# Performance work log

Measured on AMD Instinct MI355X. Metric: run time of the kernel, lower is better.

The kernel has to match this reference:

```python
import jax, jax.numpy as jnp
import numpy as np

B, S, D = 2, 2048, 2048
E, K, F = 8, 2, 4096
EPS_LN = 1e-5
EPS_AUX = 1e-9


def setup_inputs() -> dict:
    key = jax.random.key(0)
    ks = jax.random.split(key, 12)
    s_d = 1.0 / np.sqrt(D)
    s_f = 1.0 / np.sqrt(F)
    return {
        "x": jax.random.normal(ks[0], (B, S, D), dtype=jnp.float32),
        # router LayerNorm
        "ln_gamma": jnp.ones((D,), jnp.float32),
        "ln_beta": jnp.zeros((D,), jnp.float32),
        # router MLP: Linear(D,D) -> ReLU -> Linear(D,E)
        "rW1": jax.random.uniform(ks[1], (D, D), jnp.float32, -s_d, s_d),
        "rb1": jnp.zeros((D,), jnp.float32),
        "rW2": jax.random.uniform(ks[2], (D, E), jnp.float32, -s_d, s_d),
        "rb2": jnp.zeros((E,), jnp.float32),
        # experts: per-expert FFN D -> F -> D
        "We1": jax.random.uniform(ks[3], (E, D, F), jnp.float32, -s_d, s_d),
        "be1": jnp.zeros((E, F), jnp.float32),
        "We2": jax.random.uniform(ks[4], (E, F, D), jnp.float32, -s_f, s_f),
        "be2": jnp.zeros((E, D), jnp.float32),
    }


def _layer_norm(x, gamma, beta):
    mu = jnp.mean(x, axis=-1, keepdims=True)
    var = jnp.mean(jnp.square(x - mu), axis=-1, keepdims=True)
    return (x - mu) * jax.lax.rsqrt(var + EPS_LN) * gamma + beta


def reference(x, ln_gamma, ln_beta, rW1, rb1, rW2, rb2, We1, be1, We2, be2):
    # --- BaseRouter ---
    x_norm = _layer_norm(x, ln_gamma, ln_beta)
    h = jax.nn.relu(jnp.einsum("bsd,de->bse", x_norm, rW1) + rb1)
    router_logits = jnp.einsum("bsd,de->bse", h, rW2) + rb2  # [B,S,E]
    router_probs = jax.nn.softmax(router_logits, axis=-1)

    top_k_probs, top_k_indices = jax.lax.top_k(router_probs, K)  # [B,S,K]
    top_k_probs = top_k_probs / jnp.sum(top_k_probs, axis=-1, keepdims=True)

    # aux load-balance loss (detached in original via .item())
    p_mean = jnp.mean(router_probs, axis=(0, 1))  # [E]
    aux_loss = jnp.sum(p_mean * jnp.log(p_mean * E + EPS_AUX))

    # --- dispatch / combine weights: scatter top-k probs to [B,S,E] ---
    one_hot = jax.nn.one_hot(top_k_indices, E, dtype=x.dtype)  # [B,S,K,E]
    combine = jnp.einsum("bske,bsk->bse", one_hot, top_k_probs)  # [B,S,E]

    # --- experts: dense per-expert FFN, weighted combine ---
    eh = jax.nn.relu(jnp.einsum("bsd,edf->ebsf", x, We1) + be1[:, None, None, :])
    ey = jnp.einsum("ebsf,efd->ebsd", eh, We2) + be2[:, None, None, :]
    out = jnp.einsum("ebsd,bse->bsd", ey, combine)

    return out, aux_loss
```

## Files before the change

kernel.cpp:

```cpp
#include <hip/hip_runtime.h>
#include <hip/hip_bf16.h>

#define NTOK 4096
#define DIM  2048
#define NEXP 8
#define FDIM 4096
#define NPAIR 8192

typedef __attribute__((ext_vector_type(4))) float     f32x4;
typedef __attribute__((ext_vector_type(8))) short     s16x8;
typedef __attribute__((ext_vector_type(4))) short     s16x4;
typedef __attribute__((ext_vector_type(8))) _Float16  f16x8;
typedef __attribute__((ext_vector_type(4))) _Float16  f16x4;

#define DEVI static __device__ __forceinline__

DEVI void gl2lds(const void* g, void* l) {
  __builtin_amdgcn_global_load_lds((const __attribute__((address_space(1))) unsigned int*)g,
                                   (__attribute__((address_space(3))) unsigned int*)l, 16, 0, 0);
}

DEVI float bf2f(unsigned short s) {
  unsigned int u = ((unsigned int)s) << 16; float f; __builtin_memcpy(&f, &u, 4); return f;
}
DEVI unsigned short f2bf(float f) {
  __hip_bfloat16 h = __float2bfloat16(f); unsigned short s; __builtin_memcpy(&s, &h, 2); return s;
}
DEVI float wredsum(float v) {
#pragma unroll
  for (int o = 32; o > 0; o >>= 1) v += __shfl_xor(v, o);
  return v;
}

__global__ __launch_bounds__(256) void ln_conv_kernel(
    const float* __restrict__ x, const float* __restrict__ gamma, const float* __restrict__ beta,
    _Float16* __restrict__ xh, _Float16* __restrict__ xl, unsigned short* __restrict__ xbf)
{
  int tok = blockIdx.x;
  int tid = threadIdx.x, lane = tid & 63, wv = tid >> 6;
  const float* xr = x + (size_t)tok * DIM;
  float v[8];
  *(float4*)(v)     = *(const float4*)(xr + tid * 8);
  *(float4*)(v + 4) = *(const float4*)(xr + tid * 8 + 4);
  float s = v[0]+v[1]+v[2]+v[3]+v[4]+v[5]+v[6]+v[7];
  __shared__ float red[4];
  s = wredsum(s);
  if (lane == 0) red[wv] = s;
  __syncthreads();
  float mu = (red[0]+red[1]+red[2]+red[3]) * (1.f / DIM);
  __syncthreads();
  float s2 = 0.f;
#pragma unroll
  for (int j = 0; j < 8; j++) { float d = v[j] - mu; s2 += d * d; }
  s2 = wredsum(s2);
  if (lane == 0) red[wv] = s2;
  __syncthreads();
  float var = (red[0]+red[1]+red[2]+red[3]) * (1.f / DIM);
  float rs = 1.0f / sqrtf(var + 1e-5f);

  float4 g0 = *(const float4*)(gamma + tid*8), g1 = *(const float4*)(gamma + tid*8 + 4);
  float4 b0 = *(const float4*)(beta  + tid*8), b1 = *(const float4*)(beta  + tid*8 + 4);
  float gg[8] = {g0.x,g0.y,g0.z,g0.w,g1.x,g1.y,g1.z,g1.w};
  float bb[8] = {b0.x,b0.y,b0.z,b0.w,b1.x,b1.y,b1.z,b1.w};
  f16x8 vh, vl; s16x8 vb;
#pragma unroll
  for (int j = 0; j < 8; j++) {
    float xn = (v[j] - mu) * rs * gg[j] + bb[j];
    _Float16 h = (_Float16)xn;
    vh[j] = h;
    vl[j] = (_Float16)((xn - (float)h) * 4096.f);
    vb[j] = (short)f2bf(v[j]);
  }
  *(f16x8*)(xh + (size_t)tok*DIM + tid*8) = vh;
  *(f16x8*)(xl + (size_t)tok*DIM + tid*8) = vl;
  *(s16x8*)(xbf + (size_t)tok*DIM + tid*8) = vb;
}

__global__ __launch_bounds__(256) void transpose_bf16_kernel(
    const float* __restrict__ src, unsigned short* __restrict__ dst, int R, int C)
{
  src += (size_t)blockIdx.z * R * C;
  dst += (size_t)blockIdx.z * R * C;
  __shared__ float tile[64][65];
  int r0 = blockIdx.y * 64, c0 = blockIdx.x * 64;
  int tx = threadIdx.x & 15, ty = threadIdx.x >> 4;
#pragma unroll
  for (int i = 0; i < 4; i++) {
    float4 v = *(const float4*)(src + (size_t)(r0 + ty*4 + i) * C + c0 + tx*4);
    tile[ty*4+i][tx*4+0] = v.x; tile[ty*4+i][tx*4+1] = v.y;
    tile[ty*4+i][tx*4+2] = v.z; tile[ty*4+i][tx*4+3] = v.w;
  }
  __syncthreads();
#pragma unroll
  for (int i = 0; i < 4; i++) {
    int c = c0 + ty*4 + i;
    s16x4 o;
    o[0] = (short)f2bf(tile[tx*4+0][ty*4+i]); o[1] = (short)f2bf(tile[tx*4+1][ty*4+i]);
    o[2] = (short)f2bf(tile[tx*4+2][ty*4+i]); o[3] = (short)f2bf(tile[tx*4+3][ty*4+i]);
    *(s16x4*)(dst + (size_t)c * R + r0 + tx*4) = o;
  }
}

__global__ __launch_bounds__(256) void transpose_f16split_kernel(
    const float* __restrict__ src, _Float16* __restrict__ dh, _Float16* __restrict__ dl, int R, int C)
{
  __shared__ float tile[64][65];
  int r0 = blockIdx.y * 64, c0 = blockIdx.x * 64;
  int tx = threadIdx.x & 15, ty = threadIdx.x >> 4;
#pragma unroll
  for (int i = 0; i < 4; i++) {
    float4 v = *(const float4*)(src + (size_t)(r0 + ty*4 + i) * C + c0 + tx*4);
    tile[ty*4+i][tx*4+0] = v.x; tile[ty*4+i][tx*4+1] = v.y;
    tile[ty*4+i][tx*4+2] = v.z; tile[ty*4+i][tx*4+3] = v.w;
  }
  __syncthreads();
#pragma unroll
  for (int i = 0; i < 4; i++) {
    int c = c0 + ty*4 + i;
    f16x4 oh, ol;
#pragma unroll
    for (int j = 0; j < 4; j++) {
      float f = tile[tx*4+j][ty*4+i];
      _Float16 h = (_Float16)f;
      oh[j] = h;
      ol[j] = (_Float16)((f - (float)h) * 4096.f);
    }
    *(f16x4*)(dh + (size_t)c * R + r0 + tx*4) = oh;
    *(f16x4*)(dl + (size_t)c * R + r0 + tx*4) = ol;
  }
}

#define R_TA 10240
#define R_TB 5120
__global__ __launch_bounds__(256) void router_gemm_kernel(
    const _Float16* __restrict__ Ah, const _Float16* __restrict__ Al,
    const _Float16* __restrict__ Bh, const _Float16* __restrict__ Bl,
    const float* __restrict__ bias, float* __restrict__ Cout)
{
  __shared__ char lds[2*R_TA + 2*R_TB];
  char* lAh = lds;             char* lAl = lds + R_TA;
  char* lBh = lds + 2*R_TA;    char* lBl = lds + 2*R_TA + R_TB;
  const int K = DIM;
  int m0 = blockIdx.y * 128, n0 = blockIdx.x * 64;
  int tid = threadIdx.x, lane = tid & 63, wv = tid >> 6;
  int wm = wv >> 1, wn = wv & 1;

  const char* srcAh[3]; const char* srcAl[3];
  const char* srcBh[2]; const char* srcBl[2];
  {
    int i = 0;
    for (int c = wv; c < 10; c += 4, i++) {
      int doff = c*1024 + lane*16;
      int row = doff / 80; int b = doff - row*80; if (b >= 64) b = 0;
      srcAh[i] = (const char*)(Ah + (size_t)(m0+row)*K) + b;
      srcAl[i] = (const char*)(Al + (size_t)(m0+row)*K) + b;
    }
    i = 0;
    for (int c = wv; c < 5; c += 4, i++) {
      int doff = c*1024 + lane*16;
      int row = doff / 80; int b = doff - row*80; if (b >= 64) b = 0;
      srcBh[i] = (const char*)(Bh + (size_t)(n0+row)*K) + b;
      srcBl[i] = (const char*)(Bl + (size_t)(n0+row)*K) + b;
    }
  }

  f32x4 acc1[4][2], acc2[4][2];
#pragma unroll
  for (int mb = 0; mb < 4; mb++)
#pragma unroll
    for (int nb = 0; nb < 2; nb++) {
      acc1[mb][nb] = (f32x4){0.f,0.f,0.f,0.f};
      acc2[mb][nb] = (f32x4){0.f,0.f,0.f,0.f};
    }

  for (int kt = 0; kt < K/32; kt++) {
    {
      int i = 0;
      for (int c = wv; c < 10; c += 4, i++) {
        gl2lds(srcAh[i], lAh + c*1024);
        gl2lds(srcAl[i], lAl + c*1024);
        srcAh[i] += 64; srcAl[i] += 64;
      }
      i = 0;
      for (int c = wv; c < 5; c += 4, i++) {
        gl2lds(srcBh[i], lBh + c*1024);
        gl2lds(srcBl[i], lBl + c*1024);
        srcBh[i] += 64; srcBl[i] += 64;
      }
    }
    __syncthreads();
    int kb = (lane >> 4) * 16;
    f16x8 ah[4], al[4], bh[2], bl[2];
#pragma unroll
    for (int mb = 0; mb < 4; mb++) {
      int r = wm*64 + mb*16 + (lane & 15);
      ah[mb] = *(const f16x8*)(lAh + r*80 + kb);
      al[mb] = *(const f16x8*)(lAl + r*80 + kb);
    }
#pragma unroll
    for (int nb = 0; nb < 2; nb++) {
      int r = wn*32 + nb*16 + (lane & 15);
      bh[nb] = *(const f16x8*)(lBh + r*80 + kb);
      bl[nb] = *(const f16x8*)(lBl + r*80 + kb);
    }
#pragma unroll
    for (int mb = 0; mb < 4; mb++)
#pragma unroll
      for (int nb = 0; nb < 2; nb++) {
        acc1[mb][nb] = __builtin_amdgcn_mfma_f32_16x16x32_f16(ah[mb], bh[nb], acc1[mb][nb], 0,0,0);
        acc2[mb][nb] = __builtin_amdgcn_mfma_f32_16x16x32_f16(ah[mb], bl[nb], acc2[mb][nb], 0,0,0);
        acc2[mb][nb] = __builtin_amdgcn_mfma_f32_16x16x32_f16(al[mb], bh[nb], acc2[mb][nb], 0,0,0);
      }
    __syncthreads();
  }
#pragma unroll
  for (int mb = 0; mb < 4; mb++)
#pragma unroll
    for (int nb = 0; nb < 2; nb++) {
      int col = n0 + wn*32 + nb*16 + (lane & 15);
      float bv = bias[col];
#pragma unroll
      for (int r = 0; r < 4; r++) {
        int m = m0 + wm*64 + mb*16 + (lane >> 4)*4 + r;
        float hval = acc1[mb][nb][r] + acc2[mb][nb][r] * (1.f/4096.f) + bv;
        Cout[(size_t)m*DIM + col] = fmaxf(hval, 0.f);
      }
    }
}

__global__ __launch_bounds__(256) void router_logits_kernel(
    const float* __restrict__ h, const float* __restrict__ rW2, const float* __restrict__ rb2,
    float* __restrict__ probs,
    int* __restrict__ eid, float* __restrict__ wts)
{
  int lane = threadIdx.x & 63, wv = threadIdx.x >> 6;
  int tok = blockIdx.x * 4 + wv;
  const float* hr = h + (size_t)tok * DIM;
  float lg[8] = {0,0,0,0,0,0,0,0};
#pragma unroll
  for (int j = 0; j < 8; j++) {
    int k = j * 256 + lane * 4;
    float4 hv = *(const float4*)(hr + k);
    float hv4[4] = {hv.x, hv.y, hv.z, hv.w};
#pragma unroll
    for (int r = 0; r < 4; r++) {
      const float4* w4 = (const float4*)(rW2 + (size_t)(k + r) * NEXP);
      float4 wa = w4[0], wb = w4[1];
      lg[0] += hv4[r]*wa.x; lg[1] += hv4[r]*wa.y; lg[2] += hv4[r]*wa.z; lg[3] += hv4[r]*wa.w;
      lg[4] += hv4[r]*wb.x; lg[5] += hv4[r]*wb.y; lg[6] += hv4[r]*wb.z; lg[7] += hv4[r]*wb.w;
    }
  }
#pragma unroll
  for (int e = 0; e < 8; e++) {
#pragma unroll
    for (int o = 32; o > 0; o >>= 1) lg[e] += __shfl_xor(lg[e], o);
  }
  if (lane == 0) {
    float l[8], p[8];
    float m = -1e30f;
#pragma unroll
    for (int e = 0; e < 8; e++) { l[e] = lg[e] + rb2[e]; m = fmaxf(m, l[e]); }
    float s = 0.f;
#pragma unroll
    for (int e = 0; e < 8; e++) { p[e] = expf(l[e] - m); s += p[e]; }
    float inv = 1.f / s;
#pragma unroll
    for (int e = 0; e < 8; e++) { p[e] *= inv; probs[(size_t)tok*8 + e] = p[e]; }
    int i0 = 0;
#pragma unroll
    for (int e = 1; e < 8; e++) if (p[e] > p[i0]) i0 = e;
    int i1 = (i0 == 0) ? 1 : 0;
#pragma unroll
    for (int e = 0; e < 8; e++) if (e != i0 && p[e] > p[i1]) i1 = e;
    float denom = 1.f / (p[i0] + p[i1]);
    eid[tok*2+0] = i0; eid[tok*2+1] = i1;
    wts[tok*2+0] = p[i0]*denom; wts[tok*2+1] = p[i1]*denom;
  }
}

__global__ __launch_bounds__(256) void router_sort_kernel(
    const int* __restrict__ eid, const float* __restrict__ probs,
    int* __restrict__ cnt, int* __restrict__ basep,
    int* __restrict__ tokenlist, int* __restrict__ pairslot,
    float* __restrict__ aux_out)
{
  __shared__ int hist[256][8];
  __shared__ float wsum[4][8];
  __shared__ int bl[8];
  __shared__ int lcnt[8];
  int t = threadIdx.x, lane = t & 63, wv = t >> 6;

  int me[32];
  {
    const int4* ep = (const int4*)(eid + t * 32);
#pragma unroll
    for (int q = 0; q < 8; q++) {
      int4 v = ep[q];
      me[q*4+0] = v.x; me[q*4+1] = v.y; me[q*4+2] = v.z; me[q*4+3] = v.w;
    }
  }
#pragma unroll
  for (int e = 0; e < 8; e++) {
    int ce = 0;
#pragma unroll
    for (int i = 0; i < 32; i++) ce += (me[i] == e) ? 1 : 0;
    hist[t][e] = ce;
  }

  float part[8] = {0,0,0,0,0,0,0,0};
  for (int i = 0; i < 16; i++) {
    const float4* p4 = (const float4*)(probs + (size_t)(t*16 + i) * 8);
    float4 a = p4[0], b = p4[1];
    part[0]+=a.x; part[1]+=a.y; part[2]+=a.z; part[3]+=a.w;
    part[4]+=b.x; part[5]+=b.y; part[6]+=b.z; part[7]+=b.w;
  }
#pragma unroll
  for (int e = 0; e < 8; e++) {
#pragma unroll
    for (int o = 32; o > 0; o >>= 1) part[e] += __shfl_xor(part[e], o);
  }
  if (lane == 0) {
#pragma unroll
    for (int e = 0; e < 8; e++) wsum[wv][e] = part[e];
  }
  __syncthreads();

  if (t < 8) {
    int running = 0;
    for (int i = 0; i < 256; i++) { int tmp = hist[i][t]; hist[i][t] = running; running += tmp; }
    lcnt[t] = running;
  }
  __syncthreads();
  if (t == 0) {
    int b = 0; float aux = 0.f;
#pragma unroll
    for (int e = 0; e < 8; e++) {
      int ce = lcnt[e];
      bl[e] = b; basep[e] = b; cnt[e] = ce; b += ce;
      float pm = (wsum[0][e]+wsum[1][e]+wsum[2][e]+wsum[3][e]) * (1.f / NTOK);
      aux += pm * logf(pm * 8.f + 1e-9f);
    }
    *aux_out = aux;
  }
  __syncthreads();

#pragma unroll
  for (int i = 0; i < 32; i++) {
    int e = me[i];
    int r = 0;
#pragma unroll
    for (int j = 0; j < i; j++) r += (me[j] == e) ? 1 : 0;
    int slot = bl[e] + hist[t][e] + r;
    int pair = t*32 + i;
    tokenlist[slot] = pair >> 1;
    pairslot[pair] = slot;
  }
}

template<int MODE>
__global__ __launch_bounds__(256, 2) void expert_gemm_v3(
    const unsigned short* __restrict__ Abase,
    const unsigned short* __restrict__ Bbase,
    const float* __restrict__ bias,
    unsigned short* __restrict__ Cout,
    const int* __restrict__ cnt, const int* __restrict__ basep,
    const int* __restrict__ tokenlist)
{
  const int K = (MODE == 1) ? DIM : FDIM;
  const int N = (MODE == 1) ? FDIM : DIM;
  __shared__ char lds[65536];
  int e = blockIdx.y >> 5, mt = blockIdx.y & 31;
  int ne = cnt[e];
  if (mt * 128 >= ne) return;
  int mbase = basep[e] + mt * 128;
  int n0 = blockIdx.x * 128;
  int tid = threadIdx.x, lane = tid & 63, wv = tid >> 6;
  int wm = wv >> 1, wn = wv & 1;

  const char* srcA[4]; const char* srcB[4];
  int sb = (((lane & 7) ^ ((lane >> 3) & 7)) << 4);
#pragma unroll
  for (int i = 0; i < 4; i++) {
    int c = wv + i*4;
    int row = c*8 + (lane >> 3);
    int slot = mbase + row; if (slot > NPAIR - 1) slot = NPAIR - 1;
    size_t arow = (MODE == 1) ? (size_t)tokenlist[slot] : (size_t)slot;
    srcA[i] = (const char*)(Abase + arow * K) + sb;
    srcB[i] = (const char*)(Bbase + ((size_t)e * N + n0 + row) * K) + sb;
  }

  f32x4 acc[4][4];
#pragma unroll
  for (int mb = 0; mb < 4; mb++)
#pragma unroll
    for (int nb = 0; nb < 4; nb++) acc[mb][nb] = (f32x4){0.f,0.f,0.f,0.f};

#pragma unroll
  for (int i = 0; i < 4; i++) {
    gl2lds(srcA[i], lds + (wv + i*4)*1024);
    gl2lds(srcB[i], lds + 16384 + (wv + i*4)*1024);
  }
  asm volatile("s_waitcnt vmcnt(0)\n\ts_barrier" ::: "memory");

  const int NT = K / 64;
  int rsw = (lane & 7) << 4;
  int cur = 0;
  for (int kt = 0; kt < NT; kt++) {
    char* cA = lds + cur*32768;
    char* cB = cA + 16384;
    if (kt + 1 < NT) {
      char* nA = lds + (cur^1)*32768;
      char* nB = nA + 16384;
      size_t ko = (size_t)(kt + 1) * 128;
#pragma unroll
      for (int i = 0; i < 4; i++) {
        gl2lds(srcA[i] + ko, nA + (wv + i*4)*1024);
        gl2lds(srcB[i] + ko, nB + (wv + i*4)*1024);
      }
    }
#pragma unroll
    for (int ks = 0; ks < 2; ks++) {
      int kb = (ks*64 + (lane >> 4)*16) ^ rsw;
      s16x8 af[4], bf[4];
#pragma unroll
      for (int mb = 0; mb < 4; mb++)
        af[mb] = *(const s16x8*)(cA + (wm*64 + mb*16 + (lane & 15))*128 + kb);
#pragma unroll
      for (int nb = 0; nb < 4; nb++)
        bf[nb] = *(const s16x8*)(cB + (wn*64 + nb*16 + (lane & 15))*128 + kb);
#pragma unroll
      for (int mb = 0; mb < 4; mb++)
#pragma unroll
        for (int nb = 0; nb < 4; nb++)
          acc[mb][nb] = __builtin_amdgcn_mfma_f32_16x16x32_bf16(af[mb], bf[nb], acc[mb][nb], 0,0,0);
    }
    __builtin_amdgcn_sched_barrier(0);
    asm volatile("s_waitcnt lgkmcnt(0)\n\ts_waitcnt vmcnt(0)\n\ts_barrier" ::: "memory");
    __builtin_amdgcn_sched_barrier(0);
    cur ^= 1;
  }

#pragma unroll
  for (int mb = 0; mb < 4; mb++)
#pragma unroll
    for (int nb = 0; nb < 4; nb++) {
      int col = n0 + wn*64 + nb*16 + (lane & 15);
      float bv = bias[(size_t)e * N + col];
#pragma unroll
      for (int r = 0; r < 4; r++) {
        int mloc = mt*128 + wm*64 + mb*16 + (lane >> 4)*4 + r;
        if (mloc < ne) {
          float v = acc[mb][nb][r] + bv;
          if (MODE == 1) v = fmaxf(v, 0.f);
          Cout[((size_t)basep[e] + mloc) * N + col] = f2bf(v);
        }
      }
    }
}

__global__ __launch_bounds__(256) void combine_kernel(
    const unsigned short* __restrict__ Yg, const int* __restrict__ pairslot,
    const float* __restrict__ wts, float* __restrict__ out)
{
  int tok = blockIdx.x, tid = threadIdx.x;
  int s0 = pairslot[tok*2], s1 = pairslot[tok*2+1];
  float w0 = wts[tok*2], w1 = wts[tok*2+1];
  s16x8 a = *(const s16x8*)(Yg + (size_t)s0 * DIM + tid*8);
  s16x8 b = *(const s16x8*)(Yg + (size_t)s1 * DIM + tid*8);
  float o[8];
#pragma unroll
  for (int j = 0; j < 8; j++)
    o[j] = w0 * bf2f((unsigned short)a[j]) + w1 * bf2f((unsigned short)b[j]);
  float* op = out + (size_t)tok * DIM + tid*8;
  float4 o0; o0.x=o[0]; o0.y=o[1]; o0.z=o[2]; o0.w=o[3];
  float4 o1; o1.x=o[4]; o1.y=o[5]; o1.z=o[6]; o1.w=o[7];
  *(float4*)op = o0;
  *(float4*)(op + 4) = o1;
}

extern "C" void kernel_launch(void* const* d_in, const int* in_sizes, int n_in,
                              void* d_out, int out_size, void* d_ws, size_t ws_size,
                              hipStream_t stream)
{
  (void)in_sizes; (void)n_in; (void)out_size; (void)ws_size;
  const float* x    = (const float*)d_in[0];
  const float* ln_g = (const float*)d_in[1];
  const float* ln_b = (const float*)d_in[2];
  const float* rW1  = (const float*)d_in[3];
  const float* rb1  = (const float*)d_in[4];
  const float* rW2  = (const float*)d_in[5];
  const float* rb2  = (const float*)d_in[6];
  const float* We1  = (const float*)d_in[7];
  const float* be1  = (const float*)d_in[8];
  const float* We2  = (const float*)d_in[9];
  const float* be2  = (const float*)d_in[10];
  float* out = (float*)d_out;
  float* aux_out = out + (size_t)NTOK * DIM;

  char* ws = (char*)d_ws;
  size_t off = 0;
  auto alloc = [&](size_t bytes) { char* p = ws + off; off += (bytes + 255) & ~(size_t)255; return p; };

  _Float16* XH   = (_Float16*)alloc((size_t)NTOK * DIM * 2);
  _Float16* XL   = (_Float16*)alloc((size_t)NTOK * DIM * 2);
  unsigned short* XBF = (unsigned short*)alloc((size_t)NTOK * DIM * 2);
  _Float16* RW1H = (_Float16*)alloc((size_t)DIM * DIM * 2);
  _Float16* RW1L = (_Float16*)alloc((size_t)DIM * DIM * 2);
  unsigned short* WET = (unsigned short*)alloc((size_t)NEXP * FDIM * DIM * 2);
  unsigned short* EH  = (unsigned short*)alloc((size_t)(NPAIR + 128) * FDIM * 2);
  char* HY = alloc((size_t)(NPAIR + 128) * DIM * 2 > (size_t)NTOK*DIM*4
                     ? (size_t)(NPAIR + 128) * DIM * 2 : (size_t)NTOK*DIM*4);
  float* H = (float*)HY;
  unsigned short* YG = (unsigned short*)HY;
  float* PROB = (float*)alloc((size_t)NTOK * 8 * 4);
  int* CNT  = (int*)alloc(256);
  int* BASE = CNT + 16;
  int* EID  = (int*)alloc((size_t)NPAIR * 4);
  float* WTS = (float*)alloc((size_t)NPAIR * 4);
  int* PAIRSLOT = (int*)alloc((size_t)NPAIR * 4);
  int* TOKLIST  = (int*)alloc((size_t)(NPAIR + 128) * 4);

  ln_conv_kernel<<<NTOK, 256, 0, stream>>>(x, ln_g, ln_b, XH, XL, XBF);
  transpose_f16split_kernel<<<dim3(DIM/64, DIM/64), 256, 0, stream>>>(rW1, RW1H, RW1L, DIM, DIM);
  transpose_bf16_kernel<<<dim3(FDIM/64, DIM/64, NEXP), 256, 0, stream>>>(We1, WET, DIM, FDIM);
  router_gemm_kernel<<<dim3(DIM/64, NTOK/128), 256, 0, stream>>>(XH, XL, RW1H, RW1L, rb1, H);
  router_logits_kernel<<<NTOK/4, 256, 0, stream>>>(H, rW2, rb2, PROB, EID, WTS);
  router_sort_kernel<<<1, 256, 0, stream>>>(EID, PROB, CNT, BASE, TOKLIST, PAIRSLOT, aux_out);
  expert_gemm_v3<1><<<dim3(FDIM/128, NEXP*32), 256, 0, stream>>>(XBF, WET, be1, EH, CNT, BASE, TOKLIST);
  transpose_bf16_kernel<<<dim3(DIM/64, FDIM/64, NEXP), 256, 0, stream>>>(We2, WET, FDIM, DIM);
  expert_gemm_v3<2><<<dim3(DIM/128, NEXP*32), 256, 0, stream>>>(EH, WET, be2, YG, CNT, BASE, TOKLIST);
  combine_kernel<<<NTOK, 256, 0, stream>>>(YG, PAIRSLOT, WTS, out);
}
```

Baseline: 838.8 us.

## Single-buffer expert GEMM LDS and raise occupancy with M-tile-fastest grid

The expert GEMM drops LDS double buffering (64KB to 32KB) and uses plain __syncthreads around each K step, with launch bounds raised to 5 waves per SIMD. The grid is reordered so M-tiles vary fastest and each expert's N-tiles fall along the y dimension. The goal is to hide latency through higher occupancy rather than in-block prefetch, and to improve weight reuse in L2 across concurrent blocks. The cost is that loads are no longer overlapped with MFMA inside a block, and the tighter register budget may spill the 64-float accumulator tile.

Result: slower. 2.153 ms (+156.7%).

```diff
diff --git a/kernel.cpp b/kernel.cpp
--- a/kernel.cpp
+++ b/kernel.cpp
@@ -358,7 +358,7 @@
 }
 
 template<int MODE>
-__global__ __launch_bounds__(256, 2) void expert_gemm_v3(
+__global__ __launch_bounds__(256, 5) void expert_gemm_v4(
     const unsigned short* __restrict__ Abase,
     const unsigned short* __restrict__ Bbase,
     const float* __restrict__ bias,
@@ -368,12 +368,14 @@
 {
   const int K = (MODE == 1) ? DIM : FDIM;
   const int N = (MODE == 1) ? FDIM : DIM;
-  __shared__ char lds[65536];
-  int e = blockIdx.y >> 5, mt = blockIdx.y & 31;
+  const int NTN = N / 128;
+  __shared__ char lds[32768];
+  int mt = blockIdx.x;
+  int e = blockIdx.y / NTN;
+  int n0 = (blockIdx.y % NTN) * 128;
   int ne = cnt[e];
   if (mt * 128 >= ne) return;
   int mbase = basep[e] + mt * 128;
-  int n0 = blockIdx.x * 128;
   int tid = threadIdx.x, lane = tid & 63, wv = tid >> 6;
   int wm = wv >> 1, wn = wv & 1;
 
@@ -395,49 +397,33 @@
 #pragma unroll
     for (int nb = 0; nb < 4; nb++) acc[mb][nb] = (f32x4){0.f,0.f,0.f,0.f};
 
-#pragma unroll
-  for (int i = 0; i < 4; i++) {
-    gl2lds(srcA[i], lds + (wv + i*4)*1024);
-    gl2lds(srcB[i], lds + 16384 + (wv + i*4)*1024);
-  }
-  asm volatile("s_waitcnt vmcnt(0)\n\ts_barrier" ::: "memory");
-
   const int NT = K / 64;
   int rsw = (lane & 7) << 4;
-  int cur = 0;
   for (int kt = 0; kt < NT; kt++) {
-    char* cA = lds + cur*32768;
-    char* cB = cA + 16384;
-    if (kt + 1 < NT) {
-      char* nA = lds + (cur^1)*32768;
-      char* nB = nA + 16384;
-      size_t ko = (size_t)(kt + 1) * 128;
-#pragma unroll
-      for (int i = 0; i < 4; i++) {
-        gl2lds(srcA[i] + ko, nA + (wv + i*4)*1024);
-        gl2lds(srcB[i] + ko, nB + (wv + i*4)*1024);
-      }
-    }
+    size_t ko = (size_t)kt * 128;
+#pragma unroll
+    for (int i = 0; i < 4; i++) {
+      gl2lds(srcA[i] + ko, lds + (wv + i*4)*1024);
+      gl2lds(srcB[i] + ko, lds + 16384 + (wv + i*4)*1024);
+    }
+    __syncthreads();
 #pragma unroll
     for (int ks = 0; ks < 2; ks++) {
       int kb = (ks*64 + (lane >> 4)*16) ^ rsw;
       s16x8 af[4], bf[4];
 #pragma unroll
       for (int mb = 0; mb < 4; mb++)
-        af[mb] = *(const s16x8*)(cA + (wm*64 + mb*16 + (lane & 15))*128 + kb);
+        af[mb] = *(const s16x8*)(lds + (wm*64 + mb*16 + (lane & 15))*128 + kb);
 #pragma unroll
       for (int nb = 0; nb < 4; nb++)
-        bf[nb] = *(const s16x8*)(cB + (wn*64 + nb*16 + (lane & 15))*128 + kb);
+        bf[nb] = *(const s16x8*)(lds + 16384 + (wn*64 + nb*16 + (lane & 15))*128 + kb);
 #pragma unroll
       for (int mb = 0; mb < 4; mb++)
 #pragma unroll
         for (int nb = 0; nb < 4; nb++)
           acc[mb][nb] = __builtin_amdgcn_mfma_f32_16x16x32_bf16(af[mb], bf[nb], acc[mb][nb], 0,0,0);
     }
-    __builtin_amdgcn_sched_barrier(0);
-    asm volatile("s_waitcnt lgkmcnt(0)\n\ts_waitcnt vmcnt(0)\n\ts_barrier" ::: "memory");
-    __builtin_amdgcn_sched_barrier(0);
-    cur ^= 1;
+    __syncthreads();
   }
 
 #pragma unroll
@@ -526,8 +512,8 @@
   router_gemm_kernel<<<dim3(DIM/64, NTOK/128), 256, 0, stream>>>(XH, XL, RW1H, RW1L, rb1, H);
   router_logits_kernel<<<NTOK/4, 256, 0, stream>>>(H, rW2, rb2, PROB, EID, WTS);
   router_sort_kernel<<<1, 256, 0, stream>>>(EID, PROB, CNT, BASE, TOKLIST, PAIRSLOT, aux_out);
-  expert_gemm_v3<1><<<dim3(FDIM/128, NEXP*32), 256, 0, stream>>>(XBF, WET, be1, EH, CNT, BASE, TOKLIST);
+  expert_gemm_v4<1><<<dim3(32, NEXP*(FDIM/128)), 256, 0, stream>>>(XBF, WET, be1, EH, CNT, BASE, TOKLIST);
   transpose_bf16_kernel<<<dim3(DIM/64, FDIM/64, NEXP), 256, 0, stream>>>(We2, WET, FDIM, DIM);
-  expert_gemm_v3<2><<<dim3(DIM/128, NEXP*32), 256, 0, stream>>>(EH, WET, be2, YG, CNT, BASE, TOKLIST);
+  expert_gemm_v4<2><<<dim3(32, NEXP*(DIM/128)), 256, 0, stream>>>(EH, WET, be2, YG, CNT, BASE, TOKLIST);
   combine_kernel<<<NTOK, 256, 0, stream>>>(YG, PAIRSLOT, WTS, out);
 }
```

## Double-buffer LDS in router GEMM to overlap global loads with MFMA

Applied to the files above, without the earlier changes.

The router GEMM now uses two LDS buffers. It prefetches the next K tile with global_load_lds while computing on the current one, where before each iteration loaded and then computed in sequence. Each iteration ends with one combined waitcnt and barrier, replacing the two syncthreads per iteration. This doubles LDS use per block, which may reduce occupancy, and it only touches the router part of the overall MoE pipeline.

Result: faster. 805.6 us, median of 3 (-4.0%).

```diff
diff --git a/kernel.cpp b/kernel.cpp
--- a/kernel.cpp
+++ b/kernel.cpp
@@ -132,14 +132,13 @@
 
 #define R_TA 10240
 #define R_TB 5120
+#define R_BUF 30720
 __global__ __launch_bounds__(256) void router_gemm_kernel(
     const _Float16* __restrict__ Ah, const _Float16* __restrict__ Al,
     const _Float16* __restrict__ Bh, const _Float16* __restrict__ Bl,
     const float* __restrict__ bias, float* __restrict__ Cout)
 {
-  __shared__ char lds[2*R_TA + 2*R_TB];
-  char* lAh = lds;             char* lAl = lds + R_TA;
-  char* lBh = lds + 2*R_TA;    char* lBl = lds + 2*R_TA + R_TB;
+  __shared__ char lds[2 * R_BUF];
   const int K = DIM;
   int m0 = blockIdx.y * 128, n0 = blockIdx.x * 64;
   int tid = threadIdx.x, lane = tid & 63, wv = tid >> 6;
@@ -164,6 +163,23 @@
     }
   }
 
+  auto stage = [&](int kt, int buf) {
+    char* base = lds + buf * R_BUF;
+    char* lAh = base;           char* lAl = base + R_TA;
+    char* lBh = base + 2*R_TA;  char* lBl = base + 2*R_TA + R_TB;
+    size_t ko = (size_t)kt * 64;
+    int i = 0;
+    for (int c = wv; c < 10; c += 4, i++) {
+      gl2lds(srcAh[i] + ko, lAh + c*1024);
+      gl2lds(srcAl[i] + ko, lAl + c*1024);
+    }
+    i = 0;
+    for (int c = wv; c < 5; c += 4, i++) {
+      gl2lds(srcBh[i] + ko, lBh + c*1024);
+      gl2lds(srcBl[i] + ko, lBl + c*1024);
+    }
+  };
+
   f32x4 acc1[4][2], acc2[4][2];
 #pragma unroll
   for (int mb = 0; mb < 4; mb++)
@@ -173,22 +189,17 @@
       acc2[mb][nb] = (f32x4){0.f,0.f,0.f,0.f};
     }
 
-  for (int kt = 0; kt < K/32; kt++) {
-    {
-      int i = 0;
-      for (int c = wv; c < 10; c += 4, i++) {
-        gl2lds(srcAh[i], lAh + c*1024);
-        gl2lds(srcAl[i], lAl + c*1024);
-        srcAh[i] += 64; srcAl[i] += 64;
-      }
-      i = 0;
-      for (int c = wv; c < 5; c += 4, i++) {
-        gl2lds(srcBh[i], lBh + c*1024);
-        gl2lds(srcBl[i], lBl + c*1024);
-        srcBh[i] += 64; srcBl[i] += 64;
-      }
-    }
-    __syncthreads();
+  stage(0, 0);
+  asm volatile("s_waitcnt vmcnt(0)\n\ts_barrier" ::: "memory");
+
+  const int NT = K / 32;
+  int cur = 0;
+  for (int kt = 0; kt < NT; kt++) {
+    char* base = lds + cur * R_BUF;
+    char* lAh = base;           char* lAl = base + R_TA;
+    char* lBh = base + 2*R_TA;  char* lBl = base + 2*R_TA + R_TB;
+    if (kt + 1 < NT) stage(kt + 1, cur ^ 1);
+
     int kb = (lane >> 4) * 16;
     f16x8 ah[4], al[4], bh[2], bl[2];
 #pragma unroll
@@ -211,7 +222,10 @@
         acc2[mb][nb] = __builtin_amdgcn_mfma_f32_16x16x32_f16(ah[mb], bl[nb], acc2[mb][nb], 0,0,0);
         acc2[mb][nb] = __builtin_amdgcn_mfma_f32_16x16x32_f16(al[mb], bh[nb], acc2[mb][nb], 0,0,0);
       }
-    __syncthreads();
+    __builtin_amdgcn_sched_barrier(0);
+    asm volatile("s_waitcnt lgkmcnt(0)\n\ts_waitcnt vmcnt(0)\n\ts_barrier" ::: "memory");
+    __builtin_amdgcn_sched_barrier(0);
+    cur ^= 1;
   }
 #pragma unroll
   for (int mb = 0; mb < 4; mb++)
```
